# Optimization experiments

Measured on AMD Instinct MI355X. Metric: run time of the kernel, lower is better.

## Reference

```python
import jax, jax.numpy as jnp
import numpy as np

D_MODEL = 1024
N_HEADS = 16
HEAD_DIM = D_MODEL // N_HEADS


def setup_inputs() -> dict:
    key = jax.random.key(0)
    kx, kq, kk, kv, ko = jax.random.split(key, 5)
    B, T = 2, 2048
    # nn.Linear(d_model, d_model, bias=False) weights, stored as [out, in] like torch
    s = 1.0 / np.sqrt(D_MODEL)
    x = jax.random.normal(kx, (B, T, D_MODEL), dtype=jnp.float32)
    Wq = jax.random.uniform(kq, (D_MODEL, D_MODEL), minval=-s, maxval=s, dtype=jnp.float32)
    Wk = jax.random.uniform(kk, (D_MODEL, D_MODEL), minval=-s, maxval=s, dtype=jnp.float32)
    Wv = jax.random.uniform(kv, (D_MODEL, D_MODEL), minval=-s, maxval=s, dtype=jnp.float32)
    Wo = jax.random.uniform(ko, (D_MODEL, D_MODEL), minval=-s, maxval=s, dtype=jnp.float32)
    return {"x": x, "Wq": Wq, "Wk": Wk, "Wv": Wv, "Wo": Wo}


def reference(x, Wq, Wk, Wv, Wo):
    B, T, C = x.shape
    H, Dh = N_HEADS, HEAD_DIM
    # projections (torch Linear: x @ W.T)
    q = (x @ Wq.T).reshape(B, T, H, Dh).transpose(0, 2, 1, 3)  # [B,H,T,Dh]
    k = (x @ Wk.T).reshape(B, T, H, Dh).transpose(0, 2, 1, 3)
    v = (x @ Wv.T).reshape(B, T, H, Dh).transpose(0, 2, 1, 3)
    scores = jnp.einsum('bhqd,bhkd->bhqk', q, k) / jnp.sqrt(jnp.float32(Dh))
    causal = jnp.tril(jnp.ones((T, T), dtype=bool))  # [T,T]
    scores = jnp.where(causal[None, None], scores, -jnp.inf)
    attn = jax.nn.softmax(scores, axis=-1)
    out = jnp.einsum('bhqk,bhkd->bhqd', attn, v)  # [B,H,T,Dh]
    out = out.transpose(0, 2, 1, 3).reshape(B, T, C)
    return out @ Wo.T
```

## Files before the change

kernel.cpp:

```cpp
#include <hip/hip_runtime.h>
#include <hip/hip_bf16.h>

#define BB 2
#define TT 2048
#define CC 1024
#define HH 16
#define DH 64

typedef __attribute__((ext_vector_type(8))) short bf16x8;
typedef __attribute__((ext_vector_type(4))) float f32x4;
using bf16 = __hip_bfloat16;

union cvt8u { bf16x8 v; bf16 b[8]; };

__device__ __forceinline__ bf16x8 load8(const bf16* p) {
    return *reinterpret_cast<const bf16x8*>(p);
}

__device__ __forceinline__ bf16x8 cvt8f(const float* p) {
    const float4 a = *reinterpret_cast<const float4*>(p);
    const float4 c = *reinterpret_cast<const float4*>(p + 4);
    cvt8u u;
    u.b[0] = __float2bfloat16(a.x); u.b[1] = __float2bfloat16(a.y);
    u.b[2] = __float2bfloat16(a.z); u.b[3] = __float2bfloat16(a.w);
    u.b[4] = __float2bfloat16(c.x); u.b[5] = __float2bfloat16(c.y);
    u.b[6] = __float2bfloat16(c.z); u.b[7] = __float2bfloat16(c.w);
    return u.v;
}

__device__ __forceinline__ f32x4 mfma16(bf16x8 a, bf16x8 b, f32x4 c) {
    return __builtin_amdgcn_mfma_f32_16x16x32_bf16(a, b, c, 0, 0, 0);
}

__device__ __forceinline__ void gload_lds16(const bf16* g, bf16* l) {
    __builtin_amdgcn_global_load_lds(
        (const __attribute__((address_space(1))) void*)g,
        (__attribute__((address_space(3))) void*)l, 16, 0, 0);
}

#define QSCALE (0.125f * 1.44269504088896f)

__global__ __launch_bounds__(256) void cvt_x(const float* __restrict__ in,
                                             bf16* __restrict__ out) {
    const int i = blockIdx.x * 256 + threadIdx.x;
    *(reinterpret_cast<bf16x8*>(out) + i) = cvt8f(in + (size_t)i * 8);
}

__global__ __launch_bounds__(256) void cvt4_w(const float* __restrict__ w0,
                                              const float* __restrict__ w1,
                                              const float* __restrict__ w2,
                                              const float* __restrict__ w3,
                                              bf16* __restrict__ out) {
    const float* in = (blockIdx.y == 0) ? w0 : (blockIdx.y == 1) ? w1
                    : (blockIdx.y == 2) ? w2 : w3;
    const int i = blockIdx.x * 256 + threadIdx.x;
    bf16* o = out + (size_t)blockIdx.y * CC * CC;
    *(reinterpret_cast<bf16x8*>(o) + i) = cvt8f(in + (size_t)i * 8);
}

template <int MODE>
__global__ __launch_bounds__(256) void gemm3(const bf16* __restrict__ A,
                                             const bf16* __restrict__ B,
                                             bf16* __restrict__ oq,
                                             bf16* __restrict__ ok,
                                             bf16* __restrict__ ov,
                                             float* __restrict__ outf) {
    __shared__ __align__(16) bf16 As[128 * 32];
    __shared__ __align__(16) bf16 Bs[128 * 32];
    const int lane = threadIdx.x & 63;
    const int wv = threadIdx.x >> 6;
    const int l15 = lane & 15;
    const int g = lane >> 4;
    const int m0 = blockIdx.x * 128;
    const int n0 = blockIdx.y * 128;

    const int srow = wv * 16 + (lane >> 2);
    const int skg = (lane & 3) * 8;
    const bf16* gA0 = A + (size_t)(m0 + srow) * CC + skg;
    const bf16* gA1 = A + (size_t)(m0 + 64 + srow) * CC + skg;
    const bf16* gB0 = B + (size_t)(n0 + srow) * CC + skg;
    const bf16* gB1 = B + (size_t)(n0 + 64 + srow) * CC + skg;
    bf16* lA0 = As + wv * 512;
    bf16* lA1 = As + 2048 + wv * 512;
    bf16* lB0 = Bs + wv * 512;
    bf16* lB1 = Bs + 2048 + wv * 512;

    const int mw = (wv >> 1) * 64;
    const int nw = (wv & 1) * 64;

    f32x4 acc[4][4] = {};

    for (int kk = 0; kk < CC; kk += 32) {
        __syncthreads();
        gload_lds16(gA0 + kk, lA0);
        gload_lds16(gA1 + kk, lA1);
        gload_lds16(gB0 + kk, lB0);
        gload_lds16(gB1 + kk, lB1);
        __syncthreads();

        bf16x8 af[4], wf[4];
#pragma unroll
        for (int mi = 0; mi < 4; mi++)
            af[mi] = load8(As + (mw + mi * 16 + l15) * 32 + g * 8);
#pragma unroll
        for (int ni = 0; ni < 4; ni++)
            wf[ni] = load8(Bs + (nw + ni * 16 + l15) * 32 + g * 8);
#pragma unroll
        for (int mi = 0; mi < 4; mi++)
#pragma unroll
            for (int ni = 0; ni < 4; ni++)
                acc[mi][ni] = mfma16(af[mi], wf[ni], acc[mi][ni]);
    }

#pragma unroll
    for (int mi = 0; mi < 4; mi++) {
#pragma unroll
        for (int ni = 0; ni < 4; ni++) {
            const int n = n0 + nw + ni * 16 + l15;
#pragma unroll
            for (int r = 0; r < 4; r++) {
                const int m = m0 + mw + mi * 16 + g * 4 + r;
                const float v = acc[mi][ni][r];
                if (MODE == 1) {
                    outf[(size_t)m * CC + n] = v;
                } else {
                    const int b = m >> 11, t = m & (TT - 1);
                    const int mat = n >> 10, nn = n & 1023;
                    const int h = nn >> 6, d = nn & 63;
                    if (mat == 0) {
                        oq[((size_t)((b * HH + h) * TT + t) << 6) + d] = __float2bfloat16(v * QSCALE);
                    } else if (mat == 1) {
                        ok[((size_t)((b * HH + h) * TT + t) << 6) + d] = __float2bfloat16(v);
                    } else {
                        ov[(size_t)((b * HH + h) * DH + d) * TT + t] = __float2bfloat16(v);
                    }
                }
            }
        }
    }
}

template <int MODE>
__global__ __launch_bounds__(256) void gemm2(const bf16* __restrict__ A,
                                             const float* __restrict__ W0,
                                             const float* __restrict__ W1,
                                             const float* __restrict__ W2,
                                             bf16* __restrict__ oq,
                                             bf16* __restrict__ ok,
                                             bf16* __restrict__ ov,
                                             float* __restrict__ outf) {
    const int lane = threadIdx.x & 63;
    const int wv = threadIdx.x >> 6;
    const int l15 = lane & 15;
    const int g = lane >> 4;
    const int mw = blockIdx.x * 128 + (wv >> 1) * 64;
    const int nw = blockIdx.y * 128 + (wv & 1) * 64;

    f32x4 acc[4][4] = {};

    const bf16* ap[4];
#pragma unroll
    for (int mi = 0; mi < 4; mi++)
        ap[mi] = A + (size_t)(mw + mi * 16 + l15) * CC + g * 8;

    const float* wfp[4];
#pragma unroll
    for (int ni = 0; ni < 4; ni++) {
        const int nt = nw + ni * 16;
        const float* base = (MODE == 1) ? W0
                          : (nt < 1024) ? W0 : (nt < 2048) ? W1 : W2;
        wfp[ni] = base + (size_t)((nt & 1023) + l15) * CC + g * 8;
    }

#pragma unroll 2
    for (int kk = 0; kk < CC; kk += 32) {
        bf16x8 af[4], wf[4];
#pragma unroll
        for (int mi = 0; mi < 4; mi++) af[mi] = load8(ap[mi] + kk);
#pragma unroll
        for (int ni = 0; ni < 4; ni++) wf[ni] = cvt8f(wfp[ni] + kk);
#pragma unroll
        for (int mi = 0; mi < 4; mi++)
#pragma unroll
            for (int ni = 0; ni < 4; ni++)
                acc[mi][ni] = mfma16(af[mi], wf[ni], acc[mi][ni]);
    }

#pragma unroll
    for (int mi = 0; mi < 4; mi++) {
#pragma unroll
        for (int ni = 0; ni < 4; ni++) {
            const int n = nw + ni * 16 + l15;
#pragma unroll
            for (int r = 0; r < 4; r++) {
                const int m = mw + mi * 16 + g * 4 + r;
                const float v = acc[mi][ni][r];
                if (MODE == 1) {
                    outf[(size_t)m * CC + n] = v;
                } else {
                    const int b = m >> 11, t = m & (TT - 1);
                    const int mat = n >> 10, nn = n & 1023;
                    const int h = nn >> 6, d = nn & 63;
                    if (mat == 0) {
                        oq[((size_t)((b * HH + h) * TT + t) << 6) + d] = __float2bfloat16(v * QSCALE);
                    } else if (mat == 1) {
                        ok[((size_t)((b * HH + h) * TT + t) << 6) + d] = __float2bfloat16(v);
                    } else {
                        ov[(size_t)((b * HH + h) * DH + d) * TT + t] = __float2bfloat16(v);
                    }
                }
            }
        }
    }
}

__global__ __launch_bounds__(128, 2) void attn_v7(const bf16* __restrict__ Q,
                                                  const bf16* __restrict__ K,
                                                  const bf16* __restrict__ Vt,
                                                  bf16* __restrict__ out) {
    __shared__ __align__(16) bf16 p_lds[2][2][16 * 72];
    __shared__ __align__(16) float o_cmb[2][4][64][4];
    __shared__ float l_cmb[2][16];
    const int lane = threadIdx.x & 63;
    const int wv = threadIdx.x >> 6;
    const int l15 = lane & 15;
    const int g = lane >> 4;

    const int bid = blockIdx.x;
    const int xcd = bid & 7;
    const int idx = bid >> 3;
    const int bh = xcd * 4 + (idx >> 6);
    const int c = idx & 63;

    const int qbA = c * 16;
    const int qbB = (127 - c) * 16;
    const int nkbA = (c >> 2) + 1;
    const int nkbB = ((127 - c) >> 2) + 1;

    const bf16* Qh = Q + (size_t)bh * TT * DH;
    const bf16* Kh = K + (size_t)bh * TT * DH;
    const bf16* Vh = Vt + (size_t)bh * DH * TT;

    const bf16x8 qa0 = load8(Qh + (size_t)(qbA + l15) * DH + g * 8);
    const bf16x8 qa1 = load8(Qh + (size_t)(qbA + l15) * DH + 32 + g * 8);
    const bf16x8 qb0 = load8(Qh + (size_t)(qbB + l15) * DH + g * 8);
    const bf16x8 qb1 = load8(Qh + (size_t)(qbB + l15) * DH + 32 + g * 8);

    f32x4 oA[4] = {}, oB[4] = {};
    float lA[4] = {0.0f, 0.0f, 0.0f, 0.0f};
    float lB[4] = {0.0f, 0.0f, 0.0f, 0.0f};

    bf16* plA = p_lds[wv][0];
    bf16* plB = p_lds[wv][1];

    bf16x8 kf0[4], kf1[4];
#pragma unroll
    for (int j = 0; j < 4; j++) {
        kf0[j] = load8(Kh + (size_t)(wv * 64 + j * 16 + l15) * DH + g * 8);
        kf1[j] = load8(Kh + (size_t)(wv * 64 + j * 16 + l15) * DH + 32 + g * 8);
    }

    for (int kb = wv; kb < nkbB; kb += 2) {
        const int k0 = kb * 64;
        const bool actA = (kb < nkbA);

        f32x4 SA[4] = {}, SB[4] = {};
        if (actA) {
#pragma unroll
            for (int j = 0; j < 4; j++) {
                SA[j] = mfma16(qa0, kf0[j], SA[j]);
                SA[j] = mfma16(qa1, kf1[j], SA[j]);
            }
        }
#pragma unroll
        for (int j = 0; j < 4; j++) {
            SB[j] = mfma16(qb0, kf0[j], SB[j]);
            SB[j] = mfma16(qb1, kf1[j], SB[j]);
        }

        bf16x8 vf0[4], vf1[4];
#pragma unroll
        for (int dt = 0; dt < 4; dt++) {
            vf0[dt] = load8(Vh + (size_t)(dt * 16 + l15) * TT + k0 + g * 8);
            vf1[dt] = load8(Vh + (size_t)(dt * 16 + l15) * TT + k0 + 32 + g * 8);
        }

        if (kb + 2 < nkbB) {
            const int kn = k0 + 128;
#pragma unroll
            for (int j = 0; j < 4; j++) {
                kf0[j] = load8(Kh + (size_t)(kn + j * 16 + l15) * DH + g * 8);
                kf1[j] = load8(Kh + (size_t)(kn + j * 16 + l15) * DH + 32 + g * 8);
            }
        }

        if (actA && kb == nkbA - 1) {
#pragma unroll
            for (int j = 0; j < 4; j++)
#pragma unroll
                for (int r = 0; r < 4; r++)
                    if (k0 + j * 16 + l15 > qbA + g * 4 + r) SA[j][r] = -1e30f;
        }
        if (kb == nkbB - 1) {
#pragma unroll
            for (int j = 0; j < 4; j++)
#pragma unroll
                for (int r = 0; r < 4; r++)
                    if (k0 + j * 16 + l15 > qbB + g * 4 + r) SB[j][r] = -1e30f;
        }

        float PA[4][4], PB[4][4];
        if (actA) {
#pragma unroll
            for (int r = 0; r < 4; r++)
#pragma unroll
                for (int j = 0; j < 4; j++) {
                    PA[j][r] = exp2f(SA[j][r]);
                    lA[r] += PA[j][r];
                }
        }
#pragma unroll
        for (int r = 0; r < 4; r++)
#pragma unroll
            for (int j = 0; j < 4; j++) {
                PB[j][r] = exp2f(SB[j][r]);
                lB[r] += PB[j][r];
            }

        if (actA) {
#pragma unroll
            for (int j = 0; j < 4; j++)
#pragma unroll
                for (int r = 0; r < 4; r++)
                    plA[(g * 4 + r) * 72 + j * 16 + l15] = __float2bfloat16(PA[j][r]);
        }
#pragma unroll
        for (int j = 0; j < 4; j++)
#pragma unroll
            for (int r = 0; r < 4; r++)
                plB[(g * 4 + r) * 72 + j * 16 + l15] = __float2bfloat16(PB[j][r]);
        asm volatile("s_waitcnt lgkmcnt(0)" ::: "memory");

        const bf16x8 pb0 = load8(plB + l15 * 72 + g * 8);
        const bf16x8 pb1 = load8(plB + l15 * 72 + 32 + g * 8);
#pragma unroll
        for (int dt = 0; dt < 4; dt++) {
            oB[dt] = mfma16(pb0, vf0[dt], oB[dt]);
            oB[dt] = mfma16(pb1, vf1[dt], oB[dt]);
        }
        if (actA) {
            const bf16x8 pa0 = load8(plA + l15 * 72 + g * 8);
            const bf16x8 pa1 = load8(plA + l15 * 72 + 32 + g * 8);
#pragma unroll
            for (int dt = 0; dt < 4; dt++) {
                oA[dt] = mfma16(pa0, vf0[dt], oA[dt]);
                oA[dt] = mfma16(pa1, vf1[dt], oA[dt]);
            }
        }
    }

#pragma unroll
    for (int xm = 1; xm < 16; xm <<= 1) {
#pragma unroll
        for (int r = 0; r < 4; r++) {
            lA[r] += __shfl_xor(lA[r], xm);
            lB[r] += __shfl_xor(lB[r], xm);
        }
    }

    if (wv == 1) {
#pragma unroll
        for (int dt = 0; dt < 4; dt++) {
            *reinterpret_cast<f32x4*>(&o_cmb[0][dt][lane][0]) = oA[dt];
            *reinterpret_cast<f32x4*>(&o_cmb[1][dt][lane][0]) = oB[dt];
        }
        if (l15 == 0) {
#pragma unroll
            for (int r = 0; r < 4; r++) {
                l_cmb[0][g * 4 + r] = lA[r];
                l_cmb[1][g * 4 + r] = lB[r];
            }
        }
    }
    __syncthreads();
    if (wv == 1) return;

#pragma unroll
    for (int dt = 0; dt < 4; dt++) {
        oA[dt] += *reinterpret_cast<const f32x4*>(&o_cmb[0][dt][lane][0]);
        oB[dt] += *reinterpret_cast<const f32x4*>(&o_cmb[1][dt][lane][0]);
    }
#pragma unroll
    for (int r = 0; r < 4; r++) {
        lA[r] += l_cmb[0][g * 4 + r];
        lB[r] += l_cmb[1][g * 4 + r];
    }

    const int b = bh >> 4, h = bh & 15;
#pragma unroll
    for (int r = 0; r < 4; r++) {
        const float invA = 1.0f / lA[r];
        const float invB = 1.0f / lB[r];
        const int tA = qbA + g * 4 + r;
        const int tB = qbB + g * 4 + r;
        bf16* opA = out + (size_t)(b * TT + tA) * CC + h * DH;
        bf16* opB = out + (size_t)(b * TT + tB) * CC + h * DH;
#pragma unroll
        for (int dt = 0; dt < 4; dt++) {
            opA[dt * 16 + l15] = __float2bfloat16(oA[dt][r] * invA);
            opB[dt * 16 + l15] = __float2bfloat16(oB[dt][r] * invB);
        }
    }
}

extern "C" void kernel_launch(void* const* d_in, const int* in_sizes, int n_in,
                              void* d_out, int out_size, void* d_ws, size_t ws_size,
                              hipStream_t stream) {
    const float* x  = (const float*)d_in[0];
    const float* Wq = (const float*)d_in[1];
    const float* Wk = (const float*)d_in[2];
    const float* Wv = (const float*)d_in[3];
    const float* Wo = (const float*)d_in[4];
    float* out = (float*)d_out;

    const size_t per = (size_t)BB * HH * TT * DH;
    bf16* Qws  = (bf16*)d_ws;
    bf16* Kws  = Qws + per;
    bf16* Vtws = Kws + per;
    bf16* xbf  = Vtws + per;
    bf16* attn = xbf;
    bf16* Wball = attn + per;
    const bool full = ws_size >= 5 * per * sizeof(bf16);

    const dim3 blk(256);
    cvt_x<<<dim3(2048), blk, 0, stream>>>(x, xbf);

    if (full) {
        cvt4_w<<<dim3(512, 4), blk, 0, stream>>>(Wq, Wk, Wv, Wo, Wball);
        gemm3<0><<<dim3(32, 24), blk, 0, stream>>>(
            xbf, Wball, Qws, Kws, Vtws, nullptr);
    } else {
        gemm2<0><<<dim3(32, 24), blk, 0, stream>>>(
            xbf, Wq, Wk, Wv, Qws, Kws, Vtws, nullptr);
    }

    attn_v7<<<dim3(2048), dim3(128), 0, stream>>>(Qws, Kws, Vtws, attn);

    if (full) {
        gemm3<1><<<dim3(32, 8), blk, 0, stream>>>(
            attn, Wball + (size_t)3 * CC * CC, nullptr, nullptr, nullptr, out);
    } else {
        gemm2<1><<<dim3(32, 8), blk, 0, stream>>>(
            attn, Wo, nullptr, nullptr, nullptr, nullptr, nullptr, out);
    }
}
```

Baseline: 240.8 us.

## Software-pipeline P·V MFMA one iteration behind with double-buffered P in LDS

The attention loop now defers the P·V matrix multiply of each key block to the next iteration. P is written to a double-buffered LDS slot, so the LDS wait and the P·V MFMAs overlap the next block's QK MFMAs and the V global loads, with a final drain after the loop. The P buffers and the cross-wave combine buffers now share one shared-memory array, separated by an added barrier. This keeps V fragments live across iterations, which raises register pressure.

```diff
diff --git a/kernel.cpp b/kernel.cpp
--- a/kernel.cpp
+++ b/kernel.cpp
@@ -214,13 +214,15 @@
     }
 }
 
-__global__ __launch_bounds__(128, 2) void attn_v7(const bf16* __restrict__ Q,
+__global__ __launch_bounds__(128, 2) void attn_v8(const bf16* __restrict__ Q,
                                                   const bf16* __restrict__ K,
                                                   const bf16* __restrict__ Vt,
                                                   bf16* __restrict__ out) {
-    __shared__ __align__(16) bf16 p_lds[2][2][16 * 72];
-    __shared__ __align__(16) float o_cmb[2][4][64][4];
-    __shared__ float l_cmb[2][16];
+    __shared__ __align__(16) char smem[18432];
+    bf16* const pbase = reinterpret_cast<bf16*>(smem);
+    float* const o_cmb = reinterpret_cast<float*>(smem);
+    float* const l_cmb = reinterpret_cast<float*>(smem + 8192);
+
     const int lane = threadIdx.x & 63;
     const int wv = threadIdx.x >> 6;
     const int l15 = lane & 15;
@@ -250,8 +252,7 @@
     float lA[4] = {0.0f, 0.0f, 0.0f, 0.0f};
     float lB[4] = {0.0f, 0.0f, 0.0f, 0.0f};
 
-    bf16* plA = p_lds[wv][0];
-    bf16* plB = p_lds[wv][1];
+    bf16* const pw = pbase + wv * 2 * 2 * 1152;
 
     bf16x8 kf0[4], kf1[4];
 #pragma unroll
@@ -260,6 +261,10 @@
         kf1[j] = load8(Kh + (size_t)(wv * 64 + j * 16 + l15) * DH + 32 + g * 8);
     }
 
+    bf16x8 vf0[4], vf1[4];
+    int par = 0;
+    bool haveP = false, prevA = false;
+
     for (int kb = wv; kb < nkbB; kb += 2) {
         const int k0 = kb * 64;
         const bool actA = (kb < nkbA);
@@ -278,7 +283,28 @@
             SB[j] = mfma16(qb1, kf1[j], SB[j]);
         }
 
-        bf16x8 vf0[4], vf1[4];
+        if (haveP) {
+            asm volatile("s_waitcnt lgkmcnt(0)" ::: "memory");
+            const bf16* rB = pw + ((par ^ 1) * 2 + 1) * 1152;
+            const bf16x8 pb0 = load8(rB + l15 * 72 + g * 8);
+            const bf16x8 pb1 = load8(rB + l15 * 72 + 32 + g * 8);
+#pragma unroll
+            for (int dt = 0; dt < 4; dt++) {
+                oB[dt] = mfma16(pb0, vf0[dt], oB[dt]);
+                oB[dt] = mfma16(pb1, vf1[dt], oB[dt]);
+            }
+            if (prevA) {
+                const bf16* rA = pw + ((par ^ 1) * 2 + 0) * 1152;
+                const bf16x8 pa0 = load8(rA + l15 * 72 + g * 8);
+                const bf16x8 pa1 = load8(rA + l15 * 72 + 32 + g * 8);
+#pragma unroll
+                for (int dt = 0; dt < 4; dt++) {
+                    oA[dt] = mfma16(pa0, vf0[dt], oA[dt]);
+                    oA[dt] = mfma16(pa1, vf1[dt], oA[dt]);
+                }
+            }
+        }
+
 #pragma unroll
         for (int dt = 0; dt < 4; dt++) {
             vf0[dt] = load8(Vh + (size_t)(dt * 16 + l15) * TT + k0 + g * 8);
@@ -309,48 +335,57 @@
                     if (k0 + j * 16 + l15 > qbB + g * 4 + r) SB[j][r] = -1e30f;
         }
 
-        float PA[4][4], PB[4][4];
         if (actA) {
 #pragma unroll
             for (int r = 0; r < 4; r++)
 #pragma unroll
                 for (int j = 0; j < 4; j++) {
-                    PA[j][r] = exp2f(SA[j][r]);
-                    lA[r] += PA[j][r];
+                    SA[j][r] = exp2f(SA[j][r]);
+                    lA[r] += SA[j][r];
                 }
         }
 #pragma unroll
         for (int r = 0; r < 4; r++)
 #pragma unroll
             for (int j = 0; j < 4; j++) {
-                PB[j][r] = exp2f(SB[j][r]);
-                lB[r] += PB[j][r];
-            }
-
+                SB[j][r] = exp2f(SB[j][r]);
+                lB[r] += SB[j][r];
+            }
+
+        bf16* wA = pw + (par * 2 + 0) * 1152;
+        bf16* wB = pw + (par * 2 + 1) * 1152;
         if (actA) {
 #pragma unroll
             for (int j = 0; j < 4; j++)
 #pragma unroll
                 for (int r = 0; r < 4; r++)
-                    plA[(g * 4 + r) * 72 + j * 16 + l15] = __float2bfloat16(PA[j][r]);
+                    wA[(g * 4 + r) * 72 + j * 16 + l15] = __float2bfloat16(SA[j][r]);
         }
 #pragma unroll
         for (int j = 0; j < 4; j++)
 #pragma unroll
             for (int r = 0; r < 4; r++)
-                plB[(g * 4 + r) * 72 + j * 16 + l15] = __float2bfloat16(PB[j][r]);
+                wB[(g * 4 + r) * 72 + j * 16 + l15] = __float2bfloat16(SB[j][r]);
+
+        par ^= 1;
+        haveP = true;
+        prevA = actA;
+    }
+
+    {
         asm volatile("s_waitcnt lgkmcnt(0)" ::: "memory");
-
-        const bf16x8 pb0 = load8(plB + l15 * 72 + g * 8);
-        const bf16x8 pb1 = load8(plB + l15 * 72 + 32 + g * 8);
+        const bf16* rB = pw + ((par ^ 1) * 2 + 1) * 1152;
+        const bf16x8 pb0 = load8(rB + l15 * 72 + g * 8);
+        const bf16x8 pb1 = load8(rB + l15 * 72 + 32 + g * 8);
 #pragma unroll
         for (int dt = 0; dt < 4; dt++) {
             oB[dt] = mfma16(pb0, vf0[dt], oB[dt]);
             oB[dt] = mfma16(pb1, vf1[dt], oB[dt]);
         }
-        if (actA) {
-            const bf16x8 pa0 = load8(plA + l15 * 72 + g * 8);
-            const bf16x8 pa1 = load8(plA + l15 * 72 + 32 + g * 8);
+        if (prevA) {
+            const bf16* rA = pw + ((par ^ 1) * 2 + 0) * 1152;
+            const bf16x8 pa0 = load8(rA + l15 * 72 + g * 8);
+            const bf16x8 pa1 = load8(rA + l15 * 72 + 32 + g * 8);
 #pragma unroll
             for (int dt = 0; dt < 4; dt++) {
                 oA[dt] = mfma16(pa0, vf0[dt], oA[dt]);
@@ -368,17 +403,19 @@
         }
     }
 
+    __syncthreads();
+
     if (wv == 1) {
 #pragma unroll
         for (int dt = 0; dt < 4; dt++) {
-            *reinterpret_cast<f32x4*>(&o_cmb[0][dt][lane][0]) = oA[dt];
-            *reinterpret_cast<f32x4*>(&o_cmb[1][dt][lane][0]) = oB[dt];
+            *reinterpret_cast<f32x4*>(&o_cmb[((0 * 4 + dt) * 64 + lane) * 4]) = oA[dt];
+            *reinterpret_cast<f32x4*>(&o_cmb[((1 * 4 + dt) * 64 + lane) * 4]) = oB[dt];
         }
         if (l15 == 0) {
 #pragma unroll
             for (int r = 0; r < 4; r++) {
-                l_cmb[0][g * 4 + r] = lA[r];
-                l_cmb[1][g * 4 + r] = lB[r];
+                l_cmb[0 * 16 + g * 4 + r] = lA[r];
+                l_cmb[1 * 16 + g * 4 + r] = lB[r];
             }
         }
     }
@@ -387,13 +424,13 @@
 
 #pragma unroll
     for (int dt = 0; dt < 4; dt++) {
-        oA[dt] += *reinterpret_cast<const f32x4*>(&o_cmb[0][dt][lane][0]);
-        oB[dt] += *reinterpret_cast<const f32x4*>(&o_cmb[1][dt][lane][0]);
+        oA[dt] += *reinterpret_cast<const f32x4*>(&o_cmb[((0 * 4 + dt) * 64 + lane) * 4]);
+        oB[dt] += *reinterpret_cast<const f32x4*>(&o_cmb[((1 * 4 + dt) * 64 + lane) * 4]);
     }
 #pragma unroll
     for (int r = 0; r < 4; r++) {
-        lA[r] += l_cmb[0][g * 4 + r];
-        lB[r] += l_cmb[1][g * 4 + r];
+        lA[r] += l_cmb[0 * 16 + g * 4 + r];
+        lB[r] += l_cmb[1 * 16 + g * 4 + r];
     }
 
     const int b = bh >> 4, h = bh & 15;
@@ -444,7 +481,7 @@
             xbf, Wq, Wk, Wv, Qws, Kws, Vtws, nullptr);
     }
 
-    attn_v7<<<dim3(2048), dim3(128), 0, stream>>>(Qws, Kws, Vtws, attn);
+    attn_v8<<<dim3(2048), dim3(128), 0, stream>>>(Qws, Kws, Vtws, attn);
 
     if (full) {
         gemm3<1><<<dim3(32, 8), blk, 0, stream>>>(
```

Result: no change. 240.8 us (-0.0%).
